# Performance work log

Hardware: AMD Instinct MI355X
Metric: run time of the kernel (lower is better)

Reference implementation:

```python
import jax, jax.numpy as jnp
import numpy as np

POI, EMB, UNITS, QDIM, B = 5000, 256, 512, 256, 64


def setup_inputs() -> dict:
    key = jax.random.key(0)
    ks = jax.random.split(key, 16)
    s = 0.05
    return {
        "x": jax.random.randint(ks[0], (B,), 0, POI),
        "query": jax.random.normal(ks[1], (B, QDIM), jnp.float32),
        "poi_embedding": jax.random.normal(ks[2], (POI, EMB), jnp.float32),
        "A_hat": jax.random.normal(ks[3], (B, B), jnp.float32),
        "dec_hidden": jax.random.normal(ks[4], (B, UNITS), jnp.float32),
        "cat_dec_hidden": jax.random.normal(ks[5], (1, B, UNITS), jnp.float32),
        # GRUCell params (keras order z, r, h; reset_after=True -> bias [2, 3*units])
        "gru_kernel": jax.random.normal(ks[6], (EMB + QDIM, 3 * UNITS), jnp.float32) * s,
        "gru_rec_kernel": jax.random.normal(ks[7], (UNITS, 3 * UNITS), jnp.float32) * s,
        "gru_bias": jax.random.normal(ks[8], (2, 3 * UNITS), jnp.float32) * s,
        # Bahdanau attention params
        "W1_w": jax.random.normal(ks[9], (EMB, UNITS), jnp.float32) * s,
        "W1_b": jnp.zeros((UNITS,), jnp.float32),
        "W2_w": jax.random.normal(ks[10], (UNITS, UNITS), jnp.float32) * s,
        "W2_b": jnp.zeros((UNITS,), jnp.float32),
        "V_w": jax.random.normal(ks[11], (UNITS, 1), jnp.float32) * s,
        "V_b": jnp.zeros((1,), jnp.float32),
        # output dense: concat(context EMB, output_ UNITS, cat_hidden UNITS) -> POI
        "fc_w": jax.random.normal(ks[12], (EMB + 2 * UNITS, POI), jnp.float32) * s,
        "fc_b": jnp.zeros((POI,), jnp.float32),
    }


def _gru_cell(x, h, kernel, rec_kernel, bias):
    # keras GRUCell, reset_after=True, gate order (z, r, h)
    xm = x @ kernel + bias[0]        # [B, 3U]
    hm = h @ rec_kernel + bias[1]    # [B, 3U]
    xz, xr, xh = jnp.split(xm, 3, axis=-1)
    hz, hr, hh = jnp.split(hm, 3, axis=-1)
    z = jax.nn.sigmoid(xz + hz)
    r = jax.nn.sigmoid(xr + hr)
    h_cand = jnp.tanh(xh + r * hh)
    h_new = z * h + (1.0 - z) * h_cand
    return h_new, h_new


def reference(x, query, poi_embedding, A_hat, dec_hidden, cat_dec_hidden,
              gru_kernel, gru_rec_kernel, gru_bias,
              W1_w, W1_b, W2_w, W2_b, V_w, V_b, fc_w, fc_b):
    emb = poi_embedding
    x1 = jnp.concatenate([emb[x], query], axis=1)          # [B, EMB+QDIM]
    output_, state = _gru_cell(x1, dec_hidden, gru_kernel, gru_rec_kernel, gru_bias)
    # Bahdanau attention: values are the full embedding table [POI, EMB]
    v_proj = emb @ W1_w + W1_b                              # [POI, U]
    q_proj = output_ @ W2_w + W2_b                          # [B, U]
    score = jnp.tanh(v_proj[None, :, :] + q_proj[:, None, :]) @ V_w + V_b  # [B, POI, 1]
    attn = jax.nn.softmax(score, axis=1)                    # [B, POI, 1]
    context = jnp.sum(attn * emb[None, :, :], axis=1)       # [B, EMB]
    out_cat = jnp.concatenate([context, output_, cat_dec_hidden[0]], axis=1)
    logits = out_cat @ fc_w + fc_b                          # [B, POI]
    return (logits, state, output_)
```

## Files before the change

### kernel.cpp

```cpp
#include <hip/hip_runtime.h>
#include <hip/hip_bf16.h>

typedef __bf16 bf16;
typedef __bf16 bf16x4 __attribute__((ext_vector_type(4)));
typedef __bf16 bf16x8 __attribute__((ext_vector_type(8)));
typedef float f32x4 __attribute__((ext_vector_type(4)));

#define BB 64
#define EMB 256
#define UNITS 512
#define POI 5000
#define KCAT 1280
#define SCLD 5024
#define LGLD 5008
#define L2E 1.4426950408889634f

__device__ __forceinline__ float rcp_(float x){ return __builtin_amdgcn_rcpf(x); }
__device__ __forceinline__ float exp2_(float x){ return __builtin_amdgcn_exp2f(x); }

__device__ __forceinline__ f32x4 mm16bt(const float* __restrict__ A, const bf16* __restrict__ Bt,
                                        int lda, int ldbk, int K, int mr, int nc,
                                        int ka, int kb, int lane){
  int q = lane >> 4;
  f32x4 acc = {0.f,0.f,0.f,0.f};
  const float* ap = A + (size_t)mr*lda + ka + q*8;
  const bf16* bp = Bt + (size_t)nc*ldbk + kb + q*8;
#pragma unroll 2
  for(int k0 = 0; k0 < K; k0 += 32){
    f32x4 a0 = *(const f32x4*)ap;
    f32x4 a1 = *(const f32x4*)(ap+4);
    bf16x8 a;
#pragma unroll
    for(int j=0;j<4;j++){ a[j] = (bf16)a0[j]; a[4+j] = (bf16)a1[j]; }
    bf16x8 b = *(const bf16x8*)bp;
    acc = __builtin_amdgcn_mfma_f32_16x16x32_bf16(a, b, acc, 0, 0, 0);
    ap += 32; bp += 32;
  }
  return acc;
}

__global__ __launch_bounds__(256) void k_tr(const float* __restrict__ fcw, const float* __restrict__ gruK,
    const float* __restrict__ gruR, const float* __restrict__ W1, const float* __restrict__ W2,
    const float* __restrict__ emb, bf16* __restrict__ fcwT, bf16* __restrict__ gKT,
    bf16* __restrict__ gRT, bf16* __restrict__ W1T, bf16* __restrict__ W2T, bf16* __restrict__ embT){
  __shared__ float ls[64][65];
  int bid = blockIdx.x, t = threadIdx.x;
  const float* src; bf16* dst; int Ks, Ns, lddst, dRows, tn, tk;
  if(bid < 1580){      src=fcw;  Ks=1280; Ns=5000; dst=fcwT; lddst=1280; dRows=5008; tn=bid/20; tk=bid%20; }
  else if(bid < 1772){ int b=bid-1580; src=gruK; Ks=512; Ns=1536; dst=gKT; lddst=512; dRows=1536; tn=b/8; tk=b%8; }
  else if(bid < 1964){ int b=bid-1772; src=gruR; Ks=512; Ns=1536; dst=gRT; lddst=512; dRows=1536; tn=b/8; tk=b%8; }
  else if(bid < 1996){ int b=bid-1964; src=W1;   Ks=256; Ns=512;  dst=W1T; lddst=256; dRows=512;  tn=b/4; tk=b%4; }
  else if(bid < 2060){ int b=bid-1996; src=W2;   Ks=512; Ns=512;  dst=W2T; lddst=512; dRows=512;  tn=b/8; tk=b%8; }
  else {               int b=bid-2060; src=emb;  Ks=5000; Ns=256; dst=embT; lddst=5056; dRows=256; tn=b/79; tk=b%79; }
  int n0 = tn*64, k0 = tk*64;
  bool fullN = (n0 + 64 <= Ns);
#pragma unroll
  for(int ps=0; ps<4; ps++){
    int r = (t>>4) + ps*16;
    int sr = k0 + r; if(sr > Ks-1) sr = Ks-1;
    int c4 = (t&15)*4;
    if(fullN){
      f32x4 v = *(const f32x4*)&src[(size_t)sr*Ns + n0 + c4];
      ls[r][c4]=v[0]; ls[r][c4+1]=v[1]; ls[r][c4+2]=v[2]; ls[r][c4+3]=v[3];
    } else {
#pragma unroll
      for(int i=0;i<4;i++){ int sc2 = n0+c4+i; if(sc2 > Ns-1) sc2 = Ns-1; ls[r][c4+i] = src[(size_t)sr*Ns + sc2]; }
    }
  }
  __syncthreads();
#pragma unroll
  for(int ps=0; ps<4; ps++){
    int rr = (t>>4) + ps*16;
    int dr = n0 + rr;
    if(dr < dRows){
      int cc = (t&15)*4;
      bf16x4 o;
#pragma unroll
      for(int i=0;i<4;i++) o[i] = (bf16)ls[cc+i][rr];
      *(bf16x4*)&dst[(size_t)dr*lddst + k0 + cc] = o;
    }
  }
}

__global__ __launch_bounds__(256) void k_gru(const int* __restrict__ x,
    const float* __restrict__ query, const float* __restrict__ emb, const float* __restrict__ h0,
    const bf16* __restrict__ gKT, const bf16* __restrict__ gRT,
    float* __restrict__ xmP, float* __restrict__ hmP){
  int lane = threadIdx.x & 63, w = threadIdx.x >> 6;
  int col = blockIdx.x*16 + (lane & 15);
  int m = w*16 + (lane & 15);
  int z = blockIdx.z;
  const float* A; const bf16* Bt; int lda, mr, ka;
  if(blockIdx.y == 0){
    Bt = gKT;
    if(z == 0){ A = emb;   mr = x[m]; lda = EMB; ka = 0; }
    else      { A = query; mr = m;    lda = 256; ka = 0; }
  } else {
    Bt = gRT; A = h0; mr = m; lda = UNITS; ka = z*256;
  }
  f32x4 acc = mm16bt(A, Bt, lda, 512, 256, mr, col, ka, z*256, lane);
  float* C = (blockIdx.y ? hmP : xmP) + (size_t)z*BB*1536;
  int rb = w*16 + (lane >> 4)*4;
#pragma unroll
  for(int r=0;r<4;r++) C[(size_t)(rb+r)*1536 + col] = acc[r];
}

__global__ void k_gates(const float* __restrict__ xmP, const float* __restrict__ hmP,
                        const float* __restrict__ bias, const float* __restrict__ h0,
                        const float* __restrict__ catd,
                        float* __restrict__ hn, float* __restrict__ outc, float* __restrict__ dout){
  int b = blockIdx.x, u = threadIdx.x;
  const float* x0 = xmP + b*1536; const float* x1s = xmP + (size_t)BB*1536 + b*1536;
  const float* h0s = hmP + b*1536; const float* h1s = hmP + (size_t)BB*1536 + b*1536;
  float xz = x0[u]      + x1s[u]      + bias[u];
  float xg = x0[512+u]  + x1s[512+u]  + bias[512+u];
  float xh = x0[1024+u] + x1s[1024+u] + bias[1024+u];
  float hz = h0s[u]      + h1s[u]      + bias[1536+u];
  float hg = h0s[512+u]  + h1s[512+u]  + bias[2048+u];
  float hh = h0s[1024+u] + h1s[1024+u] + bias[2560+u];
  float z = rcp_(1.f + exp2_(-L2E*(xz+hz)));
  float r = rcp_(1.f + exp2_(-L2E*(xg+hg)));
  float ca = xh + r*hh;
  ca = fminf(fmaxf(ca, -15.f), 15.f);
  float e = exp2_(2.f*L2E*ca);
  float hc = (e - 1.f)*rcp_(e + 1.f);
  float h = h0[b*512+u];
  float v = z*h + (1.f - z)*hc;
  hn[b*512+u] = v;
  outc[b*KCAT + 256 + u] = v;
  outc[b*KCAT + 768 + u] = catd[(size_t)b*512 + u];
  dout[(size_t)POI*BB + (size_t)b*512 + u] = v;
  dout[(size_t)POI*BB + (size_t)BB*512 + (size_t)b*512 + u] = v;
}

__global__ __launch_bounds__(64) void k_qproj(const float* __restrict__ hn, const bf16* __restrict__ W2T,
                        const float* __restrict__ W2b, float* __restrict__ Eq){
  int lane = threadIdx.x;
  int m0 = (blockIdx.x & 3)*16;
  int col = (blockIdx.x >> 2)*16 + (lane & 15);
  f32x4 acc = mm16bt(hn, W2T, UNITS, UNITS, UNITS, m0 + (lane & 15), col, 0, 0, lane);
  float bn = W2b[col];
  int rb = m0 + (lane >> 4)*4;
#pragma unroll
  for(int r=0;r<4;r++){
    float v = (acc[r] + bn)*(2.f*L2E);
    Eq[(rb+r)*UNITS + col] = exp2_(fminf(fmaxf(v, -28.f), 28.f));
  }
}

__global__ __launch_bounds__(256) void k_vscore(const float* __restrict__ emb, const bf16* __restrict__ W1T,
    const float* __restrict__ W1b, const float* __restrict__ Eq,
    const float* __restrict__ Vw, float* __restrict__ scS){
  __shared__ float evs[16][132];
  __shared__ float Qs[64][68];
  __shared__ float vws[128];
  int t = threadIdx.x, lane = t & 63, w = t >> 6;
  int p0 = blockIdx.x*16, uh = blockIdx.y*128;
  int mr = p0 + (lane & 15); if(mr > POI-1) mr = POI-1;
#pragma unroll
  for(int i=0;i<2;i++){
    int ncl = (w + i*4)*16 + (lane & 15);
    f32x4 acc = mm16bt(emb, W1T, EMB, EMB, EMB, mr, uh + ncl, 0, 0, lane);
    float bn = W1b[uh + ncl];
    int rb = (lane >> 4)*4;
#pragma unroll
    for(int r=0;r<4;r++){
      float v = (acc[r] + bn)*(2.f*L2E);
      evs[rb+r][ncl] = exp2_(fminf(fmaxf(v, -28.f), 28.f));
    }
  }
  if(t < 128) vws[t] = Vw[uh + t];
  int tp = t & 7, tb = t >> 3;
  float s00=0.f, s01=0.f, s10=0.f, s11=0.f;
  for(int c=0;c<2;c++){
    __syncthreads();
    int ub = c*64;
    for(int i=t;i<4096;i+=256){ int b=i>>6, u=i&63; Qs[b][u] = Eq[b*UNITS + uh + ub + u]; }
    __syncthreads();
#pragma unroll
    for(int u4=0;u4<16;u4++){
      f32x4 e0 = *(f32x4*)&evs[2*tp][ub+u4*4];
      f32x4 e1 = *(f32x4*)&evs[2*tp+1][ub+u4*4];
      f32x4 q0 = *(f32x4*)&Qs[2*tb][u4*4];
      f32x4 q1 = *(f32x4*)&Qs[2*tb+1][u4*4];
      f32x4 w4 = *(f32x4*)&vws[ub+u4*4];
#pragma unroll
      for(int e=0;e<4;e++){
        float wv = w4[e];
        s00 += wv * rcp_(e0[e]*q0[e] + 1.f);
        s01 += wv * rcp_(e0[e]*q1[e] + 1.f);
        s10 += wv * rcp_(e1[e]*q0[e] + 1.f);
        s11 += wv * rcp_(e1[e]*q1[e] + 1.f);
      }
    }
  }
  float* s = scS + (size_t)blockIdx.y*BB*SCLD;
  int pA = p0 + 2*tp, bA = 2*tb;
  if(pA < POI)  { s[(size_t)bA*SCLD + pA]   = s00; s[(size_t)(bA+1)*SCLD + pA]   = s01; }
  if(pA+1 < POI){ s[(size_t)bA*SCLD + pA+1] = s10; s[(size_t)(bA+1)*SCLD + pA+1] = s11; }
}

__global__ __launch_bounds__(1024) void k_softmax(float* __restrict__ sc, float* __restrict__ outc){
  __shared__ float red[1024];
  int b = blockIdx.x, t = threadIdx.x;
  if(t < 256) outc[b*KCAT + t] = 0.f;
  float* sA = sc + (size_t)b*SCLD;
  float sum = 0.f;
  for(int p=t;p<POI;p+=1024){
    float a = sA[p] + sA[(size_t)BB*SCLD + p] + sA[(size_t)2*BB*SCLD + p] + sA[(size_t)3*BB*SCLD + p];
    float wv = exp2_(-2.f*L2E*a);
    sA[p] = wv;
    sum += wv;
  }
  red[t] = sum; __syncthreads();
  for(int o=512;o>0;o>>=1){ if(t<o) red[t]+=red[t+o]; __syncthreads(); }
  float iv = rcp_(red[0]);
  for(int p=t;p<POI;p+=1024) sA[p] *= iv;
  if(t < SCLD-POI) sA[POI + t] = 0.f;
}

__global__ __launch_bounds__(256) void k_ctx(const float* __restrict__ wb, const bf16* __restrict__ embT,
                                             float* __restrict__ outc){
  int lane = threadIdx.x & 63, w = threadIdx.x >> 6;
  int n = blockIdx.x*16 + (lane & 15);
  int ky = blockIdx.y;
  int kbeg = ky*384, kk = (ky == 12) ? 416 : 384;
  f32x4 acc = mm16bt(wb, embT, SCLD, 5056, kk, w*16 + (lane & 15), n, kbeg, kbeg, lane);
  int rb = w*16 + (lane >> 4)*4;
#pragma unroll
  for(int r=0;r<4;r++) atomicAdd(&outc[(size_t)(rb+r)*KCAT + n], acc[r]);
}

__global__ __launch_bounds__(256) void k_logits(const float* __restrict__ A, const bf16* __restrict__ fcwT,
                                                float* __restrict__ lgP){
  int lane = threadIdx.x & 63, w = threadIdx.x >> 6;
  int n = blockIdx.x*16 + (lane & 15);
  int ky = blockIdx.y, kbeg = ky*640;
  f32x4 acc = mm16bt(A, fcwT, KCAT, 1280, 640, w*16 + (lane & 15), n, kbeg, kbeg, lane);
  float* dst = lgP + (size_t)ky*BB*SCLD;
  int rb = w*16 + (lane >> 4)*4;
#pragma unroll
  for(int r=0;r<4;r++) dst[(size_t)(rb+r)*LGLD + n] = acc[r];
}

__global__ __launch_bounds__(256) void k_lred(const float* __restrict__ lgP, const float* __restrict__ fcb,
                                              float* __restrict__ out){
  int idx = blockIdx.x*256 + threadIdx.x;
  int m = idx / 1252, nq = idx % 1252;
  int n = nq*4;
  if(n < POI){
    f32x4 a = *(const f32x4*)&lgP[(size_t)m*LGLD + n];
    f32x4 b = *(const f32x4*)&lgP[(size_t)BB*SCLD + (size_t)m*LGLD + n];
    f32x4 c = *(const f32x4*)&fcb[n];
    f32x4 r = a + b + c;
    *(f32x4*)&out[(size_t)m*POI + n] = r;
  }
}

extern "C" void kernel_launch(void* const* d_in, const int* in_sizes, int n_in,
                              void* d_out, int out_size, void* d_ws, size_t ws_size,
                              hipStream_t stream){
  const int*   x     = (const int*)d_in[0];
  const float* query = (const float*)d_in[1];
  const float* emb   = (const float*)d_in[2];
  const float* h0    = (const float*)d_in[4];
  const float* catd  = (const float*)d_in[5];
  const float* gruK  = (const float*)d_in[6];
  const float* gruR  = (const float*)d_in[7];
  const float* gruB  = (const float*)d_in[8];
  const float* W1    = (const float*)d_in[9];
  const float* W1b   = (const float*)d_in[10];
  const float* W2    = (const float*)d_in[11];
  const float* W2b   = (const float*)d_in[12];
  const float* Vw    = (const float*)d_in[13];
  const float* fcw   = (const float*)d_in[15];
  const float* fcb   = (const float*)d_in[16];
  float* out = (float*)d_out;

  char* ws = (char*)d_ws;
  size_t off = 0;
  auto alloc = [&](size_t bytes)->void*{ void* p = ws + off; off += (bytes + 255) & ~(size_t)255; return p; };
  float* outc = (float*)alloc((size_t)BB*KCAT*4);
  float* xmP  = (float*)alloc((size_t)2*BB*1536*4);
  float* hmP  = (float*)alloc((size_t)2*BB*1536*4);
  float* hn   = (float*)alloc((size_t)BB*512*4);
  float* Eq   = (float*)alloc((size_t)BB*512*4);
  float* sc   = (float*)alloc((size_t)4*BB*SCLD*4);
  bf16* fcwT  = (bf16*)alloc((size_t)5008*1280*2);
  bf16* gKT   = (bf16*)alloc((size_t)1536*512*2);
  bf16* gRT   = (bf16*)alloc((size_t)1536*512*2);
  bf16* W1T   = (bf16*)alloc((size_t)512*256*2);
  bf16* W2T   = (bf16*)alloc((size_t)512*512*2);
  bf16* embT  = (bf16*)alloc((size_t)256*5056*2);
  float* lgP  = sc + (size_t)BB*SCLD;

  k_tr     <<<2376, 256, 0, stream>>>(fcw, gruK, gruR, W1, W2, emb, fcwT, gKT, gRT, W1T, W2T, embT);
  k_gru    <<<dim3(96,2,2), 256, 0, stream>>>(x, query, emb, h0, gKT, gRT, xmP, hmP);
  k_gates  <<<BB, 512, 0, stream>>>(xmP, hmP, gruB, h0, catd, hn, outc, out);
  k_qproj  <<<128, 64, 0, stream>>>(hn, W2T, W2b, Eq);
  k_vscore <<<dim3(313,4), 256, 0, stream>>>(emb, W1T, W1b, Eq, Vw, sc);
  k_softmax<<<BB, 1024, 0, stream>>>(sc, outc);
  k_ctx    <<<dim3(16,13), 256, 0, stream>>>(sc, embT, outc);
  k_logits <<<dim3(313,2), 256, 0, stream>>>(outc, fcwT, lgP);
  k_lred   <<<313, 256, 0, stream>>>(lgP, fcb, out);
}
```

Baseline: 214.5 us.

## Fuse GRU matmul into transpose kernel, atomic logits epilogue, pairwise reciprocal in vscore

The GRU input and recurrent matmuls are moved into the weight-transpose kernel as extra blocks. They read the fp32 weights directly with strided loads, so they no longer wait on the transposed copies and one launch disappears. The split-K logits reduction kernel is replaced by atomicAdd into the output, which k_gates now zeroes first, and the bias is added by the first K slice. In the attention score loop, pairs of reciprocals are merged into one reciprocal of a product to cut rcp instructions, at the cost of a few extra FMAs and some rounding or overflow risk.

```diff
diff --git a/kernel.cpp b/kernel.cpp
--- a/kernel.cpp
+++ b/kernel.cpp
@@ -12,12 +12,31 @@
 #define POI 5000
 #define KCAT 1280
 #define SCLD 5024
-#define LGLD 5008
 #define L2E 1.4426950408889634f
 
 __device__ __forceinline__ float rcp_(float x){ return __builtin_amdgcn_rcpf(x); }
 __device__ __forceinline__ float exp2_(float x){ return __builtin_amdgcn_exp2f(x); }
 
+__device__ __forceinline__ f32x4 mm16f(const float* __restrict__ A, const float* __restrict__ B,
+                                       int lda, int ldb, int K, int mr, int nc, int lane){
+  int q = lane >> 4;
+  f32x4 acc = {0.f,0.f,0.f,0.f};
+  const float* ap = A + (size_t)mr*lda + q*8;
+  const float* bp = B + (size_t)(q*8)*ldb + nc;
+#pragma unroll 2
+  for(int k0 = 0; k0 < K; k0 += 32){
+    f32x4 a0 = *(const f32x4*)ap;
+    f32x4 a1 = *(const f32x4*)(ap+4);
+    bf16x8 a, b;
+#pragma unroll
+    for(int j=0;j<4;j++){ a[j] = (bf16)a0[j]; a[4+j] = (bf16)a1[j]; }
+#pragma unroll
+    for(int j=0;j<8;j++) b[j] = (bf16)bp[(size_t)j*ldb];
+    acc = __builtin_amdgcn_mfma_f32_16x16x32_bf16(a, b, acc, 0, 0, 0);
+    ap += 32; bp += (size_t)32*ldb;
+  }
+  return acc;
+}
 __device__ __forceinline__ f32x4 mm16bt(const float* __restrict__ A, const bf16* __restrict__ Bt,
                                         int lda, int ldbk, int K, int mr, int nc,
                                         int ka, int kb, int lane){
@@ -39,70 +58,71 @@
   return acc;
 }
 
-__global__ __launch_bounds__(256) void k_tr(const float* __restrict__ fcw, const float* __restrict__ gruK,
+__global__ __launch_bounds__(256) void k_trgru(const float* __restrict__ fcw, const float* __restrict__ gruK,
     const float* __restrict__ gruR, const float* __restrict__ W1, const float* __restrict__ W2,
     const float* __restrict__ emb, bf16* __restrict__ fcwT, bf16* __restrict__ gKT,
-    bf16* __restrict__ gRT, bf16* __restrict__ W1T, bf16* __restrict__ W2T, bf16* __restrict__ embT){
-  __shared__ float ls[64][65];
+    bf16* __restrict__ gRT, bf16* __restrict__ W1T, bf16* __restrict__ W2T, bf16* __restrict__ embT,
+    const int* __restrict__ x, const float* __restrict__ query, const float* __restrict__ h0,
+    float* __restrict__ xmP, float* __restrict__ hmP){
   int bid = blockIdx.x, t = threadIdx.x;
-  const float* src; bf16* dst; int Ks, Ns, lddst, dRows, tn, tk;
-  if(bid < 1580){      src=fcw;  Ks=1280; Ns=5000; dst=fcwT; lddst=1280; dRows=5008; tn=bid/20; tk=bid%20; }
-  else if(bid < 1772){ int b=bid-1580; src=gruK; Ks=512; Ns=1536; dst=gKT; lddst=512; dRows=1536; tn=b/8; tk=b%8; }
-  else if(bid < 1964){ int b=bid-1772; src=gruR; Ks=512; Ns=1536; dst=gRT; lddst=512; dRows=1536; tn=b/8; tk=b%8; }
-  else if(bid < 1996){ int b=bid-1964; src=W1;   Ks=256; Ns=512;  dst=W1T; lddst=256; dRows=512;  tn=b/4; tk=b%4; }
-  else if(bid < 2060){ int b=bid-1996; src=W2;   Ks=512; Ns=512;  dst=W2T; lddst=512; dRows=512;  tn=b/8; tk=b%8; }
-  else {               int b=bid-2060; src=emb;  Ks=5000; Ns=256; dst=embT; lddst=5056; dRows=256; tn=b/79; tk=b%79; }
-  int n0 = tn*64, k0 = tk*64;
-  bool fullN = (n0 + 64 <= Ns);
-#pragma unroll
-  for(int ps=0; ps<4; ps++){
-    int r = (t>>4) + ps*16;
-    int sr = k0 + r; if(sr > Ks-1) sr = Ks-1;
-    int c4 = (t&15)*4;
-    if(fullN){
-      f32x4 v = *(const f32x4*)&src[(size_t)sr*Ns + n0 + c4];
-      ls[r][c4]=v[0]; ls[r][c4+1]=v[1]; ls[r][c4+2]=v[2]; ls[r][c4+3]=v[3];
+  if(bid < 2376){
+    __shared__ float ls[64][65];
+    const float* src; bf16* dst; int Ks, Ns, lddst, dRows, tn, tk;
+    if(bid < 1580){      src=fcw;  Ks=1280; Ns=5000; dst=fcwT; lddst=1280; dRows=5008; tn=bid/20; tk=bid%20; }
+    else if(bid < 1772){ int b=bid-1580; src=gruK; Ks=512; Ns=1536; dst=gKT; lddst=512; dRows=1536; tn=b/8; tk=b%8; }
+    else if(bid < 1964){ int b=bid-1772; src=gruR; Ks=512; Ns=1536; dst=gRT; lddst=512; dRows=1536; tn=b/8; tk=b%8; }
+    else if(bid < 1996){ int b=bid-1964; src=W1;   Ks=256; Ns=512;  dst=W1T; lddst=256; dRows=512;  tn=b/4; tk=b%4; }
+    else if(bid < 2060){ int b=bid-1996; src=W2;   Ks=512; Ns=512;  dst=W2T; lddst=512; dRows=512;  tn=b/8; tk=b%8; }
+    else {               int b=bid-2060; src=emb;  Ks=5000; Ns=256; dst=embT; lddst=5056; dRows=256; tn=b/79; tk=b%79; }
+    int n0 = tn*64, k0 = tk*64;
+    bool fullN = (n0 + 64 <= Ns);
+#pragma unroll
+    for(int ps=0; ps<4; ps++){
+      int r = (t>>4) + ps*16;
+      int sr = k0 + r; if(sr > Ks-1) sr = Ks-1;
+      int c4 = (t&15)*4;
+      if(fullN){
+        f32x4 v = *(const f32x4*)&src[(size_t)sr*Ns + n0 + c4];
+        ls[r][c4]=v[0]; ls[r][c4+1]=v[1]; ls[r][c4+2]=v[2]; ls[r][c4+3]=v[3];
+      } else {
+#pragma unroll
+        for(int i=0;i<4;i++){ int sc2 = n0+c4+i; if(sc2 > Ns-1) sc2 = Ns-1; ls[r][c4+i] = src[(size_t)sr*Ns + sc2]; }
+      }
+    }
+    __syncthreads();
+#pragma unroll
+    for(int ps=0; ps<4; ps++){
+      int rr = (t>>4) + ps*16;
+      int dr = n0 + rr;
+      if(dr < dRows){
+        int cc = (t&15)*4;
+        bf16x4 o;
+#pragma unroll
+        for(int i=0;i<4;i++) o[i] = (bf16)ls[cc+i][rr];
+        *(bf16x4*)&dst[(size_t)dr*lddst + k0 + cc] = o;
+      }
+    }
+  } else {
+    int g = bid - 2376;
+    int lane = t & 63, w = t >> 6;
+    int bx = g % 96, rem = g / 96, by = rem & 1, z = rem >> 1;
+    int col = bx*16 + (lane & 15);
+    int m = w*16 + (lane & 15);
+    const float* A; const float* B; int lda, mr;
+    if(by == 0){
+      B = gruK + (size_t)(z*256)*1536;
+      if(z == 0){ A = emb;   mr = x[m]; lda = EMB; }
+      else      { A = query; mr = m;    lda = 256; }
     } else {
-#pragma unroll
-      for(int i=0;i<4;i++){ int sc2 = n0+c4+i; if(sc2 > Ns-1) sc2 = Ns-1; ls[r][c4+i] = src[(size_t)sr*Ns + sc2]; }
-    }
-  }
-  __syncthreads();
-#pragma unroll
-  for(int ps=0; ps<4; ps++){
-    int rr = (t>>4) + ps*16;
-    int dr = n0 + rr;
-    if(dr < dRows){
-      int cc = (t&15)*4;
-      bf16x4 o;
-#pragma unroll
-      for(int i=0;i<4;i++) o[i] = (bf16)ls[cc+i][rr];
-      *(bf16x4*)&dst[(size_t)dr*lddst + k0 + cc] = o;
-    }
-  }
-}
-
-__global__ __launch_bounds__(256) void k_gru(const int* __restrict__ x,
-    const float* __restrict__ query, const float* __restrict__ emb, const float* __restrict__ h0,
-    const bf16* __restrict__ gKT, const bf16* __restrict__ gRT,
-    float* __restrict__ xmP, float* __restrict__ hmP){
-  int lane = threadIdx.x & 63, w = threadIdx.x >> 6;
-  int col = blockIdx.x*16 + (lane & 15);
-  int m = w*16 + (lane & 15);
-  int z = blockIdx.z;
-  const float* A; const bf16* Bt; int lda, mr, ka;
-  if(blockIdx.y == 0){
-    Bt = gKT;
-    if(z == 0){ A = emb;   mr = x[m]; lda = EMB; ka = 0; }
-    else      { A = query; mr = m;    lda = 256; ka = 0; }
-  } else {
-    Bt = gRT; A = h0; mr = m; lda = UNITS; ka = z*256;
-  }
-  f32x4 acc = mm16bt(A, Bt, lda, 512, 256, mr, col, ka, z*256, lane);
-  float* C = (blockIdx.y ? hmP : xmP) + (size_t)z*BB*1536;
-  int rb = w*16 + (lane >> 4)*4;
-#pragma unroll
-  for(int r=0;r<4;r++) C[(size_t)(rb+r)*1536 + col] = acc[r];
+      B = gruR + (size_t)(z*256)*1536;
+      A = h0 + z*256; mr = m; lda = UNITS;
+    }
+    f32x4 acc = mm16f(A, B, lda, 1536, 256, mr, col, lane);
+    float* C = (by ? hmP : xmP) + (size_t)z*BB*1536;
+    int rb = w*16 + (lane >> 4)*4;
+#pragma unroll
+    for(int r=0;r<4;r++) C[(size_t)(rb+r)*1536 + col] = acc[r];
+  }
 }
 
 __global__ void k_gates(const float* __restrict__ xmP, const float* __restrict__ hmP,
@@ -110,6 +130,7 @@
                         const float* __restrict__ catd,
                         float* __restrict__ hn, float* __restrict__ outc, float* __restrict__ dout){
   int b = blockIdx.x, u = threadIdx.x;
+  for(int p=u;p<POI;p+=512) dout[(size_t)b*POI + p] = 0.f;
   const float* x0 = xmP + b*1536; const float* x1s = xmP + (size_t)BB*1536 + b*1536;
   const float* h0s = hmP + b*1536; const float* h1s = hmP + (size_t)BB*1536 + b*1536;
   float xz = x0[u]      + x1s[u]      + bias[u];
@@ -185,12 +206,18 @@
       f32x4 q1 = *(f32x4*)&Qs[2*tb+1][u4*4];
       f32x4 w4 = *(f32x4*)&vws[ub+u4*4];
 #pragma unroll
-      for(int e=0;e<4;e++){
-        float wv = w4[e];
-        s00 += wv * rcp_(e0[e]*q0[e] + 1.f);
-        s01 += wv * rcp_(e0[e]*q1[e] + 1.f);
-        s10 += wv * rcp_(e1[e]*q0[e] + 1.f);
-        s11 += wv * rcp_(e1[e]*q1[e] + 1.f);
+      for(int h=0;h<2;h++){
+        int i0 = 2*h, i1 = i0+1;
+        float w0 = w4[i0], w1 = w4[i1];
+        float da, db;
+        da = __builtin_fmaf(e0[i0], q0[i0], 1.f); db = __builtin_fmaf(e0[i1], q0[i1], 1.f);
+        s00 = __builtin_fmaf(__builtin_fmaf(w0, db, w1*da), rcp_(da*db), s00);
+        da = __builtin_fmaf(e0[i0], q1[i0], 1.f); db = __builtin_fmaf(e0[i1], q1[i1], 1.f);
+        s01 = __builtin_fmaf(__builtin_fmaf(w0, db, w1*da), rcp_(da*db), s01);
+        da = __builtin_fmaf(e1[i0], q0[i0], 1.f); db = __builtin_fmaf(e1[i1], q0[i1], 1.f);
+        s10 = __builtin_fmaf(__builtin_fmaf(w0, db, w1*da), rcp_(da*db), s10);
+        da = __builtin_fmaf(e1[i0], q1[i0], 1.f); db = __builtin_fmaf(e1[i1], q1[i1], 1.f);
+        s11 = __builtin_fmaf(__builtin_fmaf(w0, db, w1*da), rcp_(da*db), s11);
       }
     }
   }
@@ -232,28 +259,17 @@
 }
 
 __global__ __launch_bounds__(256) void k_logits(const float* __restrict__ A, const bf16* __restrict__ fcwT,
-                                                float* __restrict__ lgP){
+                        const float* __restrict__ fcb, float* __restrict__ out){
   int lane = threadIdx.x & 63, w = threadIdx.x >> 6;
   int n = blockIdx.x*16 + (lane & 15);
+  int nc = n < POI ? n : POI-1;
   int ky = blockIdx.y, kbeg = ky*640;
-  f32x4 acc = mm16bt(A, fcwT, KCAT, 1280, 640, w*16 + (lane & 15), n, kbeg, kbeg, lane);
-  float* dst = lgP + (size_t)ky*BB*SCLD;
+  f32x4 acc = mm16bt(A, fcwT, KCAT, 1280, 640, w*16 + (lane & 15), nc, kbeg, kbeg, lane);
   int rb = w*16 + (lane >> 4)*4;
-#pragma unroll
-  for(int r=0;r<4;r++) dst[(size_t)(rb+r)*LGLD + n] = acc[r];
-}
-
-__global__ __launch_bounds__(256) void k_lred(const float* __restrict__ lgP, const float* __restrict__ fcb,
-                                              float* __restrict__ out){
-  int idx = blockIdx.x*256 + threadIdx.x;
-  int m = idx / 1252, nq = idx % 1252;
-  int n = nq*4;
   if(n < POI){
-    f32x4 a = *(const f32x4*)&lgP[(size_t)m*LGLD + n];
-    f32x4 b = *(const f32x4*)&lgP[(size_t)BB*SCLD + (size_t)m*LGLD + n];
-    f32x4 c = *(const f32x4*)&fcb[n];
-    f32x4 r = a + b + c;
-    *(f32x4*)&out[(size_t)m*POI + n] = r;
+    float bn = (ky == 0) ? fcb[n] : 0.f;
+#pragma unroll
+    for(int r=0;r<4;r++) atomicAdd(&out[(size_t)(rb+r)*POI + n], acc[r] + bn);
   }
 }
 
@@ -292,15 +308,13 @@
   bf16* W1T   = (bf16*)alloc((size_t)512*256*2);
   bf16* W2T   = (bf16*)alloc((size_t)512*512*2);
   bf16* embT  = (bf16*)alloc((size_t)256*5056*2);
-  float* lgP  = sc + (size_t)BB*SCLD;
-
-  k_tr     <<<2376, 256, 0, stream>>>(fcw, gruK, gruR, W1, W2, emb, fcwT, gKT, gRT, W1T, W2T, embT);
-  k_gru    <<<dim3(96,2,2), 256, 0, stream>>>(x, query, emb, h0, gKT, gRT, xmP, hmP);
+
+  k_trgru  <<<2760, 256, 0, stream>>>(fcw, gruK, gruR, W1, W2, emb, fcwT, gKT, gRT, W1T, W2T, embT,
+                                      x, query, h0, xmP, hmP);
   k_gates  <<<BB, 512, 0, stream>>>(xmP, hmP, gruB, h0, catd, hn, outc, out);
   k_qproj  <<<128, 64, 0, stream>>>(hn, W2T, W2b, Eq);
   k_vscore <<<dim3(313,4), 256, 0, stream>>>(emb, W1T, W1b, Eq, Vw, sc);
   k_softmax<<<BB, 1024, 0, stream>>>(sc, outc);
   k_ctx    <<<dim3(16,13), 256, 0, stream>>>(sc, embT, outc);
-  k_logits <<<dim3(313,2), 256, 0, stream>>>(outc, fcwT, lgP);
-  k_lred   <<<313, 256, 0, stream>>>(lgP, fcb, out);
-}
+  k_logits <<<dim3(313,2), 256, 0, stream>>>(outc, fcwT, fcb, out);
+}
```

New measurement: 214.3 us. About the same (-0.1%).
